# Performance work log

Measured on AMD Instinct MI355X. Metric: run time of the kernel, lower is better.

The kernel has to match this reference:

```python
import math
import jax, jax.numpy as jnp
import numpy as np

D_MODEL = 256
D2 = 2 * D_MODEL
NHEADS = 8
NLAYERS = 6
FFN = 1024
Q, B, S = 300, 16, 1024


def _ln(x, eps=1e-5):
    m = jnp.mean(x, axis=-1, keepdims=True)
    v = jnp.mean((x - m) ** 2, axis=-1, keepdims=True)
    return (x - m) / jnp.sqrt(v + eps)


def _mlp2(x, W1, b1, W2, b2):
    return jnp.maximum(x @ W1 + b1, 0.0) @ W2 + b2


def _sine_embed(pos, d_model):
    # pos: [Q, B, 2] -> [Q, B, d_model]
    fd = d_model // 2
    dim_t = jnp.arange(fd, dtype=jnp.float32)
    dim_t = 10000.0 ** (2.0 * jnp.floor(dim_t / 2.0) / fd)
    scale = 2.0 * math.pi
    px = (pos[:, :, 0] * scale)[:, :, None] / dim_t
    py = (pos[:, :, 1] * scale)[:, :, None] / dim_t

    def inter(p):
        q, b, _ = p.shape
        return jnp.stack((jnp.sin(p[:, :, 0::2]), jnp.cos(p[:, :, 1::2])), axis=3).reshape(q, b, -1)

    return jnp.concatenate((inter(py), inter(px)), axis=2)


def _pairwise_iou(b):
    # b: [B, Q, 4] xyxy -> [B, Q, Q]
    area = (b[..., 2] - b[..., 0]) * (b[..., 3] - b[..., 1])
    lt = jnp.maximum(b[:, :, None, :2], b[:, None, :, :2])
    rb = jnp.minimum(b[:, :, None, 2:], b[:, None, :, 2:])
    wh = jnp.clip(rb - lt, 0.0)
    inter = wh[..., 0] * wh[..., 1]
    union = area[:, :, None] + area[:, None, :] - inter
    return inter / union


def _mha(q, k, v, Wq, Wk, Wv, Wo, bias=None):
    # q: [L,B,D], k/v: [S,B,D]
    L, Bb, D = q.shape
    Ss = k.shape[0]
    hd = D // NHEADS
    qh = (q @ Wq).reshape(L, Bb, NHEADS, hd).transpose(1, 2, 0, 3)  # [B,H,L,hd]
    kh = (k @ Wk).reshape(Ss, Bb, NHEADS, hd).transpose(1, 2, 0, 3)
    vh = (v @ Wv).reshape(Ss, Bb, NHEADS, hd).transpose(1, 2, 0, 3)
    logits = jnp.einsum('bhqd,bhkd->bhqk', qh, kh) / jnp.sqrt(jnp.float32(hd))
    if bias is not None:
        logits = logits + bias[:, None]  # broadcast over heads
    a = jax.nn.softmax(logits, axis=-1)
    o = jnp.einsum('bhqk,bhkd->bhqd', a, vh).transpose(2, 0, 1, 3).reshape(L, Bb, D)
    return o @ Wo


def setup_inputs() -> dict:
    key = jax.random.key(0)
    ks = iter(jax.random.split(key, 40))
    f32 = jnp.float32
    d = D_MODEL
    sc = 0.02
    inp = {
        'tgt': jax.random.normal(next(ks), (Q, B, D2), f32),
        'memory': jax.random.normal(next(ks), (S, B, D2), f32),
        'pos': jax.random.normal(next(ks), (S, B, D2), f32),
        'query_pos': jax.random.normal(next(ks), (Q, B, d), f32),
        # query_scale MLP (d->d->d)
        'qs_W1': jax.random.normal(next(ks), (d, d), f32) * sc, 'qs_b1': jnp.zeros((d,), f32),
        'qs_W2': jax.random.normal(next(ks), (d, d), f32) * sc, 'qs_b2': jnp.zeros((d,), f32),
        # ref_point_head MLP (d->d->2)
        'rp_W1': jax.random.normal(next(ks), (d, d), f32) * sc, 'rp_b1': jnp.zeros((d,), f32),
        'rp_W2': jax.random.normal(next(ks), (d, 2), f32) * sc, 'rp_b2': jnp.zeros((2,), f32),
        # bbox_embed_func MLP (d->d->4)
        'bb_W1': jax.random.normal(next(ks), (d, d), f32) * sc, 'bb_b1': jnp.zeros((d,), f32),
        'bb_W2': jax.random.normal(next(ks), (d, 4), f32) * sc, 'bb_b2': jnp.zeros((4,), f32),
    }
    for name in ['sa_Wq', 'sa_Wk', 'sa_Wv', 'sa_Wo', 'ca_Wq', 'ca_Wk', 'ca_Wv', 'ca_Wo']:
        inp[name] = jax.random.normal(next(ks), (NLAYERS, D2, D2), f32) * sc
    inp['ff_W1'] = jax.random.normal(next(ks), (NLAYERS, D2, FFN), f32) * sc
    inp['ff_b1'] = jnp.zeros((NLAYERS, FFN), f32)
    inp['ff_W2'] = jax.random.normal(next(ks), (NLAYERS, FFN, D2), f32) * sc
    inp['ff_b2'] = jnp.zeros((NLAYERS, D2), f32)
    return inp


def reference(tgt, memory, pos, query_pos,
              qs_W1, qs_b1, qs_W2, qs_b2,
              rp_W1, rp_b1, rp_W2, rp_b2,
              bb_W1, bb_b1, bb_W2, bb_b2,
              sa_Wq, sa_Wk, sa_Wv, sa_Wo,
              ca_Wq, ca_Wk, ca_Wv, ca_Wo,
              ff_W1, ff_b1, ff_W2, ff_b2):
    d = D_MODEL
    output = tgt
    ref_before = _mlp2(query_pos, rp_W1, rp_b1, rp_W2, rp_b2)          # [Q,B,2]
    reference_points = jax.nn.sigmoid(ref_before).transpose(1, 0, 2)   # [B,Q,2]
    qp2 = jnp.concatenate((query_pos, query_pos), axis=-1)             # [Q,B,2d]
    for l in range(NLAYERS):
        obj_center = reference_points.transpose(1, 0, 2)               # [Q,B,2]
        pos_transform = _mlp2(output[..., d:], qs_W1, qs_b1, qs_W2, qs_b2)
        qs = _sine_embed(obj_center, d) * pos_transform                # [Q,B,d]
        tmp = _mlp2(output[..., d:], bb_W1, bb_b1, bb_W2, bb_b2)       # [Q,B,4]
        tmp = tmp.at[..., :2].add(ref_before)
        coord = jax.nn.sigmoid(tmp)                                    # cxcywh
        cx, cy, w, h = coord[..., 0], coord[..., 1], coord[..., 2], coord[..., 3]
        boxes = jnp.stack((cx - 0.5 * w, cy - 0.5 * h, cx + 0.5 * w, cy + 0.5 * h),
                          axis=-1).transpose(1, 0, 2)                  # [B,Q,4]
        gious = jax.lax.stop_gradient(_pairwise_iou(boxes))            # [B,Q,Q]
        cs = (cx + cy).transpose(1, 0)                                 # [B,Q]
        cxcys = jax.lax.stop_gradient((cs[:, :, None] > cs[:, None, :]).astype(output.dtype))
        bias = gious + cxcys                                            # [B,Q,Q]
        qs2 = jnp.concatenate((qs, qs), axis=-1)                        # [Q,B,2d]
        # self-attention with giou/cxcy bias
        qsa = output + qp2
        sa = _mha(qsa, qsa, output, sa_Wq[l], sa_Wk[l], sa_Wv[l], sa_Wo[l], bias=bias)
        output = _ln(output + sa)
        # cross-attention, sine-modulated query
        ca = _mha(output + qp2 + qs2, memory + pos, memory,
                  ca_Wq[l], ca_Wk[l], ca_Wv[l], ca_Wo[l])
        output = _ln(output + ca)
        ff = jnp.maximum(output @ ff_W1[l] + ff_b1[l], 0.0) @ ff_W2[l] + ff_b2[l]
        output = _ln(output + ff)
    return output[None]  # [1,Q,B,2d]
```

## Files before the change

kernel.cpp:

```cpp
#include <hip/hip_runtime.h>
#include <cmath>

#define QLEN 300
#define BATCH 16
#define SLEN 1024
#define DM 256
#define DD 512
#define FFND 1024
#define NQROWS (QLEN*BATCH)
#define NMROWS (SLEN*BATCH)
#define LQPAD 304
#define SAKPAD 320

typedef __attribute__((ext_vector_type(8))) short short8;
typedef __attribute__((ext_vector_type(4))) float f32x4;
typedef __attribute__((ext_vector_type(4))) unsigned short ushort4_;

__device__ __forceinline__ float sigmoidf_(float x){ return 1.f/(1.f+expf(-x)); }

__device__ __forceinline__ unsigned short f2bf(float x){
  unsigned u = __float_as_uint(x);
  unsigned r = (u + 0x7FFFu + ((u >> 16) & 1u)) >> 16;
  return (unsigned short)r;
}
__device__ __forceinline__ float bf2f(unsigned short u){
  return __uint_as_float(((unsigned)u) << 16);
}

__device__ __forceinline__ void gload16(const void* g, void* l) {
  __builtin_amdgcn_global_load_lds((const __attribute__((address_space(1))) unsigned int*)g,
                                   (__attribute__((address_space(3))) unsigned int*)l, 16, 0, 0);
}

__global__ __launch_bounds__(256) void transpose_cvt(
    const float* __restrict__ W, unsigned short* __restrict__ Wt, int K, int N,
    size_t zsrc, size_t zdst, float scale)
{
  __shared__ float T[32][33];
  int n0 = blockIdx.x*32, k0 = blockIdx.y*32;
  size_t zs = (size_t)blockIdx.z * zsrc;
  size_t zd = (size_t)blockIdx.z * zdst;
  int tx = threadIdx.x & 31, ty = threadIdx.x >> 5;
  #pragma unroll
  for (int j = 0; j < 32; j += 8)
    T[ty+j][tx] = W[zs + (size_t)(k0+ty+j)*N + n0+tx];
  __syncthreads();
  #pragma unroll
  for (int j = 0; j < 32; j += 8)
    Wt[zd + (size_t)(n0+ty+j)*K + k0+tx] = f2bf(T[tx][ty+j] * scale);
}

__global__ void concat_bias(const float* __restrict__ b1, const float* __restrict__ b2,
                            float* __restrict__ out)
{
  int i = blockIdx.x*256 + threadIdx.x;
  if (i < 256) out[i] = b1[i];
  else if (i < 512) out[i] = b2[i-256];
}

template<int BM, int OUTMODE, bool RELU>
__global__ __launch_bounds__(256) void gemm2(
    const unsigned short* __restrict__ Ab, const unsigned short* __restrict__ Wt,
    const float* __restrict__ bias, void* __restrict__ Cptr,
    int M, int N, int K, int lda, int Laux)
{
  __shared__ __align__(16) unsigned short As[2][BM*64];
  __shared__ __align__(16) unsigned short Bs[2][128*64];
  const int tid = threadIdx.x;
  const int w = tid >> 6, lane = tid & 63;
  const int bm = blockIdx.y*BM, bn = blockIdx.x*128;
  const int wm = w >> 1, wn = w & 1;
  const int c = lane & 15, hi = lane >> 4;
  constexpr int MR = (BM + 31)/32 < 1 ? 1 : BM/32;
  f32x4 acc[MR < 1 ? 1 : MR][4] = {};
  const int lrow8 = lane >> 3;
  const int lcol  = ((lane & 7) ^ lrow8) << 3;
  const int nt = K >> 6;

  auto stage = [&](int buf, int k0) {
    #pragma unroll
    for (int it = 0; it < BM/32; ++it) {
      int r = it*32 + w*8;
      gload16(&Ab[(size_t)(bm + r + lrow8)*lda + k0 + lcol], &As[buf][r*64]);
    }
    #pragma unroll
    for (int it = 0; it < 4; ++it) {
      int r = it*32 + w*8;
      gload16(&Wt[(size_t)(bn + r + lrow8)*K + k0 + lcol], &Bs[buf][r*64]);
    }
  };

  stage(0, 0);
  for (int t = 0; t < nt; ++t) {
    const int cur = t & 1;
    if (t + 1 < nt) {
      stage(cur ^ 1, (t+1) << 6);
      if constexpr (BM == 32)      asm volatile("s_waitcnt vmcnt(5)" ::: "memory");
      else if constexpr (BM == 64) asm volatile("s_waitcnt vmcnt(6)" ::: "memory");
      else                         asm volatile("s_waitcnt vmcnt(8)" ::: "memory");
    } else {
      asm volatile("s_waitcnt vmcnt(0)" ::: "memory");
    }
    __builtin_amdgcn_s_barrier();
    #pragma unroll
    for (int ks = 0; ks < 2; ++ks) {
      short8 a[MR], bf[4];
      #pragma unroll
      for (int mr = 0; mr < MR; ++mr) {
        int m = wm*(BM/2) + mr*16 + c;
        a[mr] = *reinterpret_cast<const short8*>(&As[cur][m*64 + ((ks*32 + hi*8) ^ ((m&7)<<3))]);
      }
      #pragma unroll
      for (int nr = 0; nr < 4; ++nr) {
        int n = wn*64 + nr*16 + c;
        bf[nr] = *reinterpret_cast<const short8*>(&Bs[cur][n*64 + ((ks*32 + hi*8) ^ ((n&7)<<3))]);
      }
      #pragma unroll
      for (int mr = 0; mr < MR; ++mr)
        #pragma unroll
        for (int nr = 0; nr < 4; ++nr)
          acc[mr][nr] = __builtin_amdgcn_mfma_f32_16x16x32_bf16(a[mr], bf[nr], acc[mr][nr], 0, 0, 0);
    }
    asm volatile("s_waitcnt lgkmcnt(0)" ::: "memory");
    __builtin_amdgcn_sched_barrier(0);
    __builtin_amdgcn_s_barrier();
  }
  const int hs = N >> 6;
  #pragma unroll
  for (int mr = 0; mr < MR; ++mr) {
    #pragma unroll
    for (int nr = 0; nr < 4; ++nr) {
      int colg = bn + wn*64 + nr*16 + c;
      float bv = bias ? bias[colg] : 0.f;
      #pragma unroll
      for (int r = 0; r < 4; ++r) {
        int rowg = bm + wm*(BM/2) + mr*16 + hi*4 + r;
        float v = acc[mr][nr][r] + bv;
        if (RELU) v = fmaxf(v, 0.f);
        if (OUTMODE == 0) {
          ((float*)Cptr)[(size_t)rowg*N + colg] = v;
        } else if (OUTMODE == 1) {
          ((unsigned short*)Cptr)[(size_t)rowg*N + colg] = f2bf(v);
        } else {
          int bb = rowg & 15, row = rowg >> 4, h = colg >> 6, dl = colg & 63;
          ((unsigned short*)Cptr)[(((size_t)bb*hs + h)*Laux + row)*64 + dl] = f2bf(v);
        }
      }
    }
  }
}

template<int BM>
__global__ __launch_bounds__(256) void gemm2_vt(
    const unsigned short* __restrict__ Ab, const unsigned short* __restrict__ Wt,
    unsigned short* __restrict__ VT, int Lsrc, int K, int lda, int Lkpad, int tilesPerB)
{
  __shared__ __align__(16) unsigned short As[2][BM*64];
  __shared__ __align__(16) unsigned short Bs[2][128*64];
  const int tid = threadIdx.x;
  const int w = tid >> 6, lane = tid & 63;
  const int b = blockIdx.y / tilesPerB;
  const int qt = (blockIdx.y - b*tilesPerB) * BM;
  const int bn = blockIdx.x*128;
  const int wm = w >> 1, wn = w & 1;
  const int c = lane & 15, hi = lane >> 4;
  constexpr int MR = BM/32;
  f32x4 acc[MR][4] = {};
  const int lrow8 = lane >> 3;
  const int lcol  = ((lane & 7) ^ lrow8) << 3;
  const int nt = K >> 6;

  auto stage = [&](int buf, int k0) {
    #pragma unroll
    for (int it = 0; it < BM/32; ++it) {
      int r = it*32 + w*8;
      int q = qt + r + lrow8; if (q > Lsrc-1) q = Lsrc-1;
      gload16(&Ab[(size_t)(q*BATCH + b)*lda + k0 + lcol], &As[buf][r*64]);
    }
    #pragma unroll
    for (int it = 0; it < 4; ++it) {
      int r = it*32 + w*8;
      gload16(&Wt[(size_t)(bn + r + lrow8)*K + k0 + lcol], &Bs[buf][r*64]);
    }
  };

  stage(0, 0);
  for (int t = 0; t < nt; ++t) {
    const int cur = t & 1;
    if (t + 1 < nt) {
      stage(cur ^ 1, (t+1) << 6);
      if constexpr (BM == 64) asm volatile("s_waitcnt vmcnt(6)" ::: "memory");
      else                    asm volatile("s_waitcnt vmcnt(8)" ::: "memory");
    } else {
      asm volatile("s_waitcnt vmcnt(0)" ::: "memory");
    }
    __builtin_amdgcn_s_barrier();
    #pragma unroll
    for (int ks = 0; ks < 2; ++ks) {
      short8 a[MR], bf[4];
      #pragma unroll
      for (int mr = 0; mr < MR; ++mr) {
        int m = wm*(BM/2) + mr*16 + c;
        a[mr] = *reinterpret_cast<const short8*>(&As[cur][m*64 + ((ks*32 + hi*8) ^ ((m&7)<<3))]);
      }
      #pragma unroll
      for (int nr = 0; nr < 4; ++nr) {
        int n = wn*64 + nr*16 + c;
        bf[nr] = *reinterpret_cast<const short8*>(&Bs[cur][n*64 + ((ks*32 + hi*8) ^ ((n&7)<<3))]);
      }
      #pragma unroll
      for (int mr = 0; mr < MR; ++mr)
        #pragma unroll
        for (int nr = 0; nr < 4; ++nr)
          acc[mr][nr] = __builtin_amdgcn_mfma_f32_16x16x32_bf16(a[mr], bf[nr], acc[mr][nr], 0, 0, 0);
    }
    asm volatile("s_waitcnt lgkmcnt(0)" ::: "memory");
    __builtin_amdgcn_sched_barrier(0);
    __builtin_amdgcn_s_barrier();
  }
  #pragma unroll
  for (int mr = 0; mr < MR; ++mr) {
    #pragma unroll
    for (int nr = 0; nr < 4; ++nr) {
      int colg = bn + wn*64 + nr*16 + c;
      int h = colg >> 6, dl = colg & 63;
      int q0 = qt + wm*(BM/2) + mr*16 + hi*4;
      ushort4_ pack;
      #pragma unroll
      for (int r = 0; r < 4; ++r) pack[r] = f2bf(acc[mr][nr][r]);
      *reinterpret_cast<ushort4_*>(&VT[((size_t)(b*8 + h)*64 + dl)*Lkpad + q0]) = pack;
    }
  }
}

__global__ __launch_bounds__(256) void gemm_mfma_split(
    const unsigned short* __restrict__ Ab, const unsigned short* __restrict__ Wt,
    const float* __restrict__ bias, unsigned short* __restrict__ C1, float* __restrict__ C2,
    int M, int N, int K, int lda)
{
  __shared__ __align__(16) unsigned short As[64][72];
  __shared__ __align__(16) unsigned short Bs[64][72];
  const int tid = threadIdx.x;
  const int bm = blockIdx.y*64, bn = blockIdx.x*64;
  const int w = tid >> 6, lane = tid & 63;
  const int wm = w >> 1, wn = w & 1;
  const int c = lane & 15, hi = lane >> 4;
  const int sr = tid >> 3, sk = (tid & 7) * 8;
  f32x4 acc[2][2] = {};
  for (int k0 = 0; k0 < K; k0 += 64) {
    #pragma unroll
    for (int it = 0; it < 2; ++it) {
      int m = sr + it*32;
      short8 v = *reinterpret_cast<const short8*>(&Ab[(size_t)(bm+m)*lda + k0 + sk]);
      *reinterpret_cast<short8*>(&As[m][sk]) = v;
      short8 bv = *reinterpret_cast<const short8*>(&Wt[(size_t)(bn+m)*K + k0 + sk]);
      *reinterpret_cast<short8*>(&Bs[m][sk]) = bv;
    }
    __syncthreads();
    #pragma unroll
    for (int ks = 0; ks < 2; ++ks) {
      short8 a0 = *reinterpret_cast<const short8*>(&As[wm*32 + c][ks*32 + hi*8]);
      short8 a1 = *reinterpret_cast<const short8*>(&As[wm*32 + 16 + c][ks*32 + hi*8]);
      short8 b0 = *reinterpret_cast<const short8*>(&Bs[wn*32 + c][ks*32 + hi*8]);
      short8 b1 = *reinterpret_cast<const short8*>(&Bs[wn*32 + 16 + c][ks*32 + hi*8]);
      acc[0][0] = __builtin_amdgcn_mfma_f32_16x16x32_bf16(a0, b0, acc[0][0], 0, 0, 0);
      acc[0][1] = __builtin_amdgcn_mfma_f32_16x16x32_bf16(a0, b1, acc[0][1], 0, 0, 0);
      acc[1][0] = __builtin_amdgcn_mfma_f32_16x16x32_bf16(a1, b0, acc[1][0], 0, 0, 0);
      acc[1][1] = __builtin_amdgcn_mfma_f32_16x16x32_bf16(a1, b1, acc[1][1], 0, 0, 0);
    }
    __syncthreads();
  }
  #pragma unroll
  for (int mf = 0; mf < 2; ++mf) {
    #pragma unroll
    for (int nf = 0; nf < 2; ++nf) {
      int colg = bn + wn*32 + nf*16 + c;
      float bv = bias[colg];
      #pragma unroll
      for (int r = 0; r < 4; ++r) {
        int rowg = bm + wm*32 + mf*16 + hi*4 + r;
        float v = fmaxf(acc[mf][nf][r] + bv, 0.f);
        if (colg < 256) C1[(size_t)rowg*256 + colg] = f2bf(v);
        else            C2[(size_t)rowg*256 + (colg-256)] = v;
      }
    }
  }
}

template<bool HAS_BIAS, bool MASK, int NS>
__global__ __launch_bounds__(256) void attn2(
    const unsigned short* __restrict__ Qh, const unsigned short* __restrict__ Kh,
    const unsigned short* __restrict__ VT, const float* __restrict__ bias,
    unsigned short* __restrict__ Ob, unsigned short* __restrict__ Opart, float* __restrict__ MLpart,
    int Lq, int Lk, int Lkpad, int qmul, int kmul, int koff)
{
  __shared__ __align__(16) unsigned short Ks[2][64*64];
  __shared__ __align__(16) unsigned short Vs[2][64*64];
  __shared__ __align__(16) unsigned short Pl[4][16*64];
  const int tid = threadIdx.x;
  const int w = tid >> 6, lane = tid & 63;
  const int c = lane & 15, hi = lane >> 4;
  const int bh = blockIdx.x;
  const int qt = blockIdx.y * 64;
  const int sp = blockIdx.z;
  const int b = bh >> 3, h = bh & 7;
  const int lrow8 = lane >> 3;
  const int lcol  = ((lane & 7) ^ lrow8) << 3;

  const int nt_tot = (Lk + 63) >> 6;
  const int t0 = (nt_tot * sp) / NS;
  const int t1 = (nt_tot * (sp + 1)) / NS;

  int qrow = qt + w*16 + c; if (qrow > Lq-1) qrow = Lq-1;
  const unsigned short* qptr = Qh + ((size_t)(b*qmul + h)*Lq + qrow)*64;
  short8 qf0 = *reinterpret_cast<const short8*>(qptr + hi*8);
  short8 qf1 = *reinterpret_cast<const short8*>(qptr + 32 + hi*8);
  const size_t kbase = (size_t)(b*kmul + koff + h)*Lk;

  float m_ = -1e30f, l_ = 0.f;
  f32x4 accO[4] = {};
  const int qbase = qt + w*16 + hi*4;

  auto stageKV = [&](int buf, int kt) {
    #pragma unroll
    for (int it = 0; it < 2; ++it) {
      int r = it*32 + w*8;
      int kr = kt + r + lrow8; if (MASK && kr > Lk-1) kr = Lk-1;
      gload16(&Kh[(kbase + kr)*64 + lcol], &Ks[buf][r*64]);
    }
    #pragma unroll
    for (int it = 0; it < 2; ++it) {
      int r = it*32 + w*8;
      gload16(&VT[((size_t)bh*64 + r + lrow8)*Lkpad + kt + lcol], &Vs[buf][r*64]);
    }
  };

  stageKV(0, t0 << 6);
  for (int t = t0; t < t1; ++t) {
    const int cur = (t - t0) & 1;
    const int kt = t << 6;
    float4 bs4[4];
    if (HAS_BIAS) {
      #pragma unroll
      for (int g = 0; g < 4; ++g)
        bs4[g] = *reinterpret_cast<const float4*>(
            &bias[((size_t)b*Lq + qrow)*Lk + kt + g*16 + hi*4]);
    }
    if (t + 1 < t1) {
      stageKV(cur ^ 1, (t+1) << 6);
      asm volatile("s_waitcnt vmcnt(4)" ::: "memory");
    } else {
      asm volatile("s_waitcnt vmcnt(0)" ::: "memory");
    }
    __builtin_amdgcn_s_barrier();
    f32x4 s[4] = {};
    __builtin_amdgcn_s_setprio(1);
    #pragma unroll
    for (int g = 0; g < 4; ++g) {
      int m = g*16 + c;
      short8 kb0 = *reinterpret_cast<const short8*>(&Ks[cur][m*64 + ((hi*8)      ^ ((m&7)<<3))]);
      short8 kb1 = *reinterpret_cast<const short8*>(&Ks[cur][m*64 + ((32 + hi*8) ^ ((m&7)<<3))]);
      s[g] = __builtin_amdgcn_mfma_f32_16x16x32_bf16(kb0, qf0, s[g], 0, 0, 0);
      s[g] = __builtin_amdgcn_mfma_f32_16x16x32_bf16(kb1, qf1, s[g], 0, 0, 0);
    }
    __builtin_amdgcn_s_setprio(0);
    float tmax = -1e30f;
    #pragma unroll
    for (int g = 0; g < 4; ++g) {
      #pragma unroll
      for (int r = 0; r < 4; ++r) {
        float v = s[g][r];
        if (HAS_BIAS) v += ((const float*)&bs4[g])[r];
        if (MASK && (kt + g*16 + hi*4 + r >= Lk)) v = -1e30f;
        s[g][r] = v;
        tmax = fmaxf(tmax, v);
      }
    }
    tmax = fmaxf(tmax, __shfl_xor(tmax, 16));
    tmax = fmaxf(tmax, __shfl_xor(tmax, 32));
    if (!__all(tmax - m_ <= 8.f)) {
      float newm = fmaxf(m_, tmax);
      float corr = __expf(m_ - newm);
      m_ = newm;
      l_ *= corr;
      float corr4[4];
      #pragma unroll
      for (int r = 0; r < 4; ++r) corr4[r] = __shfl(corr, hi*4 + r);
      #pragma unroll
      for (int dg = 0; dg < 4; ++dg)
        #pragma unroll
        for (int r = 0; r < 4; ++r) accO[dg][r] *= corr4[r];
    }
    float psum = 0.f;
    #pragma unroll
    for (int g = 0; g < 4; ++g) {
      ushort4_ pp;
      #pragma unroll
      for (int r = 0; r < 4; ++r) {
        float e = __expf(s[g][r] - m_);
        psum += e;
        pp[r] = f2bf(e);
      }
      int idx = c*64 + ((((g<<1)|(hi>>1)) ^ (c&7))<<3) + ((hi&1)<<2);
      *reinterpret_cast<ushort4_*>(&Pl[w][idx]) = pp;
    }
    psum += __shfl_xor(psum, 16);
    psum += __shfl_xor(psum, 32);
    l_ += psum;
    __builtin_amdgcn_s_setprio(1);
    #pragma unroll
    for (int ks = 0; ks < 2; ++ks) {
      short8 pa = *reinterpret_cast<const short8*>(&Pl[w][c*64 + ((((ks<<2)|hi) ^ (c&7))<<3)]);
      #pragma unroll
      for (int dg = 0; dg < 4; ++dg) {
        int n = dg*16 + c;
        short8 vb = *reinterpret_cast<const short8*>(&Vs[cur][n*64 + ((ks*32 + hi*8) ^ ((n&7)<<3))]);
        accO[dg] = __builtin_amdgcn_mfma_f32_16x16x32_bf16(pa, vb, accO[dg], 0, 0, 0);
      }
    }
    __builtin_amdgcn_s_setprio(0);
    asm volatile("s_waitcnt lgkmcnt(0)" ::: "memory");
    __builtin_amdgcn_sched_barrier(0);
    __builtin_amdgcn_s_barrier();
  }
  if (NS == 1) {
    float l4[4];
    #pragma unroll
    for (int r = 0; r < 4; ++r) l4[r] = __shfl(l_, hi*4 + r);
    #pragma unroll
    for (int r = 0; r < 4; ++r) {
      int qg = qbase + r;
      if (qg < Lq) {
        float inv = 1.f / l4[r];
        #pragma unroll
        for (int dg = 0; dg < 4; ++dg)
          Ob[((size_t)qg*BATCH + b)*DD + h*64 + 16*dg + c] = f2bf(accO[dg][r] * inv);
      }
    }
  } else {
    int qc = qt + w*16 + c;
    if (hi == 0 && qc < Lq) {
      size_t rowml = ((size_t)sp*128 + bh)*LQPAD + qc;
      MLpart[rowml*2]     = m_;
      MLpart[rowml*2 + 1] = l_;
    }
    #pragma unroll
    for (int r = 0; r < 4; ++r) {
      int qg = qbase + r;
      if (qg < Lq) {
        size_t rowo = ((size_t)sp*128 + bh)*LQPAD + qg;
        #pragma unroll
        for (int dg = 0; dg < 4; ++dg)
          Opart[rowo*64 + dg*16 + c] = f2bf(accO[dg][r]);
      }
    }
  }
}

template<int NSR>
__global__ __launch_bounds__(256) void attn_reduce(
    const unsigned short* __restrict__ Opart, const float* __restrict__ MLpart,
    unsigned short* __restrict__ Ob, int Lq)
{
  int w = threadIdx.x >> 6, lane = threadIdx.x & 63;
  int pair = blockIdx.x*4 + w;
  if (pair >= 128*Lq) return;
  int bh = pair / Lq, q = pair - bh*Lq;
  size_t rr[NSR];
  float m[NSR], l[NSR], M = -1e30f;
  #pragma unroll
  for (int s = 0; s < NSR; ++s) {
    rr[s] = ((size_t)s*128 + bh)*LQPAD + q;
    m[s] = MLpart[rr[s]*2];
    l[s] = MLpart[rr[s]*2 + 1];
    M = fmaxf(M, m[s]);
  }
  float o = 0.f, L = 0.f;
  #pragma unroll
  for (int s = 0; s < NSR; ++s) {
    float wg = __expf(m[s] - M);
    o += wg * bf2f(Opart[rr[s]*64 + lane]);
    L += wg * l[s];
  }
  int b = bh >> 3, h = bh & 7;
  Ob[((size_t)q*BATCH + b)*DD + h*64 + lane] = f2bf(o / L);
}

__global__ __launch_bounds__(256) void gemm_f32(
    const float* __restrict__ A, const float* __restrict__ A2,
    const float* __restrict__ W, const float* __restrict__ bias,
    float* __restrict__ C, int M, int N, int K, int lda, int relu)
{
  __shared__ __align__(16) float As[16][68];
  __shared__ __align__(16) float Bs[16][68];
  const int tid = threadIdx.x;
  const int bm = blockIdx.y * 64, bn = blockIdx.x * 64;
  const int tx = tid & 15, ty = tid >> 4;
  const int ar = tid >> 4, ac = tid & 15;
  const int bk = tid >> 6, bnn = tid & 63;
  float acc[4][4] = {};
  for (int k0 = 0; k0 < K; k0 += 16) {
    #pragma unroll
    for (int i = 0; i < 4; ++i) {
      int row = ar + i*16;
      float v = A[(size_t)(bm+row)*lda + (k0+ac)];
      if (A2) v += A2[(size_t)(bm+row)*lda + (k0+ac)];
      As[ac][row] = v;
    }
    #pragma unroll
    for (int i = 0; i < 4; ++i) {
      int kk = bk + i*4;
      Bs[kk][bnn] = W[(size_t)(k0+kk)*N + (bn+bnn)];
    }
    __syncthreads();
    #pragma unroll
    for (int k = 0; k < 16; ++k) {
      float4 a4 = *reinterpret_cast<const float4*>(&As[k][ty*4]);
      float4 b4 = *reinterpret_cast<const float4*>(&Bs[k][tx*4]);
      float a[4] = {a4.x,a4.y,a4.z,a4.w};
      float bb[4] = {b4.x,b4.y,b4.z,b4.w};
      #pragma unroll
      for (int i=0;i<4;++i)
        #pragma unroll
        for (int j=0;j<4;++j)
          acc[i][j] = fmaf(a[i], bb[j], acc[i][j]);
    }
    __syncthreads();
  }
  float vb[4] = {0.f,0.f,0.f,0.f};
  if (bias) {
    float4 b4 = *reinterpret_cast<const float4*>(&bias[bn + tx*4]);
    vb[0]=b4.x; vb[1]=b4.y; vb[2]=b4.z; vb[3]=b4.w;
  }
  #pragma unroll
  for (int i=0;i<4;++i) {
    int row = bm + ty*4 + i;
    float r0 = acc[i][0]+vb[0], r1 = acc[i][1]+vb[1], r2 = acc[i][2]+vb[2], r3 = acc[i][3]+vb[3];
    if (relu){ r0=fmaxf(r0,0.f); r1=fmaxf(r1,0.f); r2=fmaxf(r2,0.f); r3=fmaxf(r3,0.f); }
    float4 o; o.x=r0; o.y=r1; o.z=r2; o.w=r3;
    *reinterpret_cast<float4*>(&C[(size_t)row*N + bn + tx*4]) = o;
  }
}

__global__ __launch_bounds__(256) void gemm_skinny(
    const float* __restrict__ A, const float* __restrict__ W, const float* __restrict__ bias,
    float* __restrict__ C, int M, int N, int K, int lda)
{
  int wid = threadIdx.x >> 6, lane = threadIdx.x & 63;
  int row = blockIdx.x * 4 + wid;
  if (row >= M) return;
  float acc[4] = {0.f,0.f,0.f,0.f};
  for (int k = lane; k < K; k += 64) {
    float av = A[(size_t)row*lda + k];
    for (int n = 0; n < N; ++n) acc[n] += av * W[(size_t)k*N + n];
  }
  for (int off = 32; off; off >>= 1)
    for (int n = 0; n < N; ++n) acc[n] += __shfl_down(acc[n], off);
  if (lane == 0)
    for (int n = 0; n < N; ++n) C[(size_t)row*N + n] = acc[n] + bias[n];
}

__global__ void sine_embed_kernel(const float* __restrict__ refb, float* __restrict__ sine)
{
  int idx = blockIdx.x*blockDim.x + threadIdx.x;
  if (idx >= NQROWS*DM) return;
  int r = idx >> 8, c = idx & 255;
  int j = c & 127;
  float coord = refb[r*2 + (c < 128 ? 1 : 0)];
  float s = sigmoidf_(coord);
  float freq = expf(-(float)(j >> 1) * (9.210340371976184f / 64.f));
  float v = s * 6.283185307179586f * freq;
  sine[idx] = (j & 1) ? cosf(v) : sinf(v);
}

__global__ void boxes_kernel(const float* __restrict__ t4, const float* __restrict__ refb,
                             float* __restrict__ boxes, float* __restrict__ cs)
{
  int idx = blockIdx.x*blockDim.x + threadIdx.x;
  if (idx >= NQROWS) return;
  int q = idx / BATCH, b = idx % BATCH;
  float cx = sigmoidf_(t4[idx*4+0] + refb[idx*2+0]);
  float cy = sigmoidf_(t4[idx*4+1] + refb[idx*2+1]);
  float w  = sigmoidf_(t4[idx*4+2]);
  float h  = sigmoidf_(t4[idx*4+3]);
  int o = b*QLEN + q;
  boxes[o*4+0] = cx - 0.5f*w;
  boxes[o*4+1] = cy - 0.5f*h;
  boxes[o*4+2] = cx + 0.5f*w;
  boxes[o*4+3] = cy + 0.5f*h;
  cs[o] = cx + cy;
}

__global__ void bias_kernel(const float* __restrict__ boxes, const float* __restrict__ cs,
                            float* __restrict__ bias)
{
  int idx = blockIdx.x*blockDim.x + threadIdx.x;
  const int QQ = QLEN*QLEN;
  if (idx >= BATCH*QQ) return;
  int b = idx / QQ, rem = idx - b*QQ;
  int i = rem / QLEN, j = rem - i*QLEN;
  float4 bi = *reinterpret_cast<const float4*>(&boxes[((size_t)b*QLEN + i)*4]);
  float4 bj = *reinterpret_cast<const float4*>(&boxes[((size_t)b*QLEN + j)*4]);
  float ai = (bi.z-bi.x)*(bi.w-bi.y);
  float aj = (bj.z-bj.x)*(bj.w-bj.y);
  float ltx = fmaxf(bi.x, bj.x), lty = fmaxf(bi.y, bj.y);
  float rbx = fminf(bi.z, bj.z), rby = fminf(bi.w, bj.w);
  float w = fmaxf(rbx-ltx, 0.f), h = fmaxf(rby-lty, 0.f);
  float inter = w*h;
  float iou = inter / (ai + aj - inter);
  bias[idx] = iou + ((cs[b*QLEN+i] > cs[b*QLEN+j]) ? 1.f : 0.f);
}

__global__ void cvt_mem(const float* __restrict__ mem, const float* __restrict__ pos,
                        unsigned short* __restrict__ mb, unsigned short* __restrict__ mvb)
{
  int i = blockIdx.x*blockDim.x + threadIdx.x;
  if (i >= NMROWS*DD/8) return;
  size_t base = (size_t)i*8;
  float4 a0 = *reinterpret_cast<const float4*>(mem+base);
  float4 a1 = *reinterpret_cast<const float4*>(mem+base+4);
  float4 p0 = *reinterpret_cast<const float4*>(pos+base);
  float4 p1 = *reinterpret_cast<const float4*>(pos+base+4);
  short8 s1, s2;
  s1[0]=(short)f2bf(a0.x+p0.x); s1[1]=(short)f2bf(a0.y+p0.y); s1[2]=(short)f2bf(a0.z+p0.z); s1[3]=(short)f2bf(a0.w+p0.w);
  s1[4]=(short)f2bf(a1.x+p1.x); s1[5]=(short)f2bf(a1.y+p1.y); s1[6]=(short)f2bf(a1.z+p1.z); s1[7]=(short)f2bf(a1.w+p1.w);
  s2[0]=(short)f2bf(a0.x); s2[1]=(short)f2bf(a0.y); s2[2]=(short)f2bf(a0.z); s2[3]=(short)f2bf(a0.w);
  s2[4]=(short)f2bf(a1.x); s2[5]=(short)f2bf(a1.y); s2[6]=(short)f2bf(a1.z); s2[7]=(short)f2bf(a1.w);
  *reinterpret_cast<short8*>(mb+base)  = s1;
  *reinterpret_cast<short8*>(mvb+base) = s2;
}

template<int EMIT>
__global__ __launch_bounds__(256) void ln_residual_t(
    float* __restrict__ X, const float* __restrict__ Y, unsigned short* __restrict__ Xb,
    const float* __restrict__ qp, const float* __restrict__ sine, const float* __restrict__ pt,
    unsigned short* __restrict__ QIN)
{
  int row = blockIdx.x, tid = threadIdx.x;
  size_t base = (size_t)row*DD;
  float v0 = X[base+tid]     + Y[base+tid];
  float v1 = X[base+tid+256] + Y[base+tid+256];
  float s = v0+v1, sq = v0*v0+v1*v1;
  for (int off = 32; off; off >>= 1) { s += __shfl_down(s,off); sq += __shfl_down(sq,off); }
  __shared__ float ss[4], ssq[4];
  int wid = tid>>6, lane = tid&63;
  if (lane==0){ ss[wid]=s; ssq[wid]=sq; }
  __syncthreads();
  if (tid==0){
    float a=ss[0]+ss[1]+ss[2]+ss[3], bsum=ssq[0]+ssq[1]+ssq[2]+ssq[3];
    float mean = a*(1.f/DD);
    float var  = bsum*(1.f/DD) - mean*mean;
    ss[0]=mean; ssq[0]=rsqrtf(fmaxf(var,0.f)+1e-5f);
  }
  __syncthreads();
  float mean = ss[0], inv = ssq[0];
  float o0 = (v0-mean)*inv, o1 = (v1-mean)*inv;
  X[base+tid]     = o0;  Xb[base+tid]     = f2bf(o0);
  X[base+tid+256] = o1;  Xb[base+tid+256] = f2bf(o1);
  if (EMIT >= 1) {
    size_t c2 = (size_t)row*256 + tid;
    float add = qp[c2];
    if (EMIT == 2) add += sine[c2]*pt[c2];
    QIN[base+tid]     = f2bf(o0 + add);
    QIN[base+tid+256] = f2bf(o1 + add);
  }
}

__global__ void init_x(const float* __restrict__ t, const float* __restrict__ qp,
                       float* __restrict__ X, unsigned short* __restrict__ Xb,
                       unsigned short* __restrict__ QIN, int n)
{
  int idx = blockIdx.x*blockDim.x + threadIdx.x;
  if (idx < n){
    float v = t[idx]; X[idx]=v; Xb[idx]=f2bf(v);
    int r = idx >> 9, c = idx & 511;
    QIN[idx] = f2bf(v + qp[(r<<8) + (c & 255)]);
  }
}

__global__ void copy_f32(const float* __restrict__ src, float* __restrict__ dst, int n)
{
  int idx = blockIdx.x*blockDim.x + threadIdx.x;
  if (idx < n) dst[idx] = src[idx];
}

extern "C" void kernel_launch(void* const* d_in, const int* in_sizes, int n_in,
                              void* d_out, int out_size, void* d_ws, size_t ws_size,
                              hipStream_t stream)
{
  const float* tgt       = (const float*)d_in[0];
  const float* memory    = (const float*)d_in[1];
  const float* pos       = (const float*)d_in[2];
  const float* query_pos = (const float*)d_in[3];
  const float* qs_W1 = (const float*)d_in[4];  const float* qs_b1 = (const float*)d_in[5];
  const float* qs_W2 = (const float*)d_in[6];  const float* qs_b2 = (const float*)d_in[7];
  const float* rp_W1 = (const float*)d_in[8];  const float* rp_b1 = (const float*)d_in[9];
  const float* rp_W2 = (const float*)d_in[10]; const float* rp_b2 = (const float*)d_in[11];
  const float* bb_W1 = (const float*)d_in[12]; const float* bb_b1 = (const float*)d_in[13];
  const float* bb_W2 = (const float*)d_in[14]; const float* bb_b2 = (const float*)d_in[15];
  const float* sa_Wq = (const float*)d_in[16]; const float* sa_Wk = (const float*)d_in[17];
  const float* sa_Wv = (const float*)d_in[18]; const float* sa_Wo = (const float*)d_in[19];
  const float* ca_Wq = (const float*)d_in[20]; const float* ca_Wk = (const float*)d_in[21];
  const float* ca_Wv = (const float*)d_in[22]; const float* ca_Wo = (const float*)d_in[23];
  const float* ff_W1 = (const float*)d_in[24]; const float* ff_b1 = (const float*)d_in[25];
  const float* ff_W2 = (const float*)d_in[26]; const float* ff_b2 = (const float*)d_in[27];

  float* F = (float*)d_ws;
  size_t o = 0;
  float* X    = F + o; o += (size_t)NQROWS*DD;
  float* RES  = F + o; o += (size_t)NQROWS*DD;
  float* SINE = F + o; o += (size_t)NQROWS*DM;
  float* PT   = F + o; o += (size_t)NQROWS*DM;
  float* BIAS = F + o; o += (size_t)BATCH*QLEN*QLEN;
  float* REFB = F + o; o += (size_t)NQROWS*2;
  float* T4   = F + o; o += (size_t)NQROWS*4;
  float* BOX  = F + o; o += (size_t)NQROWS*4;
  float* CS   = F + o; o += (size_t)NQROWS;
  float* ML   = F + o; o += (size_t)2*128*LQPAD*2;
  float* QBB  = F + o; o += 512;
  float* T256 = RES;
  unsigned short* U = (unsigned short*)(F + o);
  size_t u = 0;
  unsigned short* Xb   = U + u; u += (size_t)NQROWS*DD;
  unsigned short* QIN  = U + u; u += (size_t)NQROWS*DD;
  unsigned short* PQb  = U + u; u += (size_t)NQROWS*DD;
  unsigned short* PKb  = U + u; u += (size_t)NMROWS*DD;
  unsigned short* PVb  = U + u; u += (size_t)NMROWS*DD;
  unsigned short* VTsa = U + u; u += (size_t)128*64*SAKPAD;
  unsigned short* OPARTU = U + u; u += (size_t)2*128*LQPAD*64;
  unsigned short* T256b= U + u; u += (size_t)NQROWS*DM;
  unsigned short* MEMb = U + u; u += (size_t)NMROWS*DD;
  unsigned short* MEMVb= U + u; u += (size_t)NMROWS*DD;
  unsigned short* WtSqk= U + u; u += (size_t)6*2*DD*DD;
  unsigned short* WtSv = U + u; u += (size_t)6*DD*DD;
  unsigned short* WtSo = U + u; u += (size_t)6*DD*DD;
  unsigned short* WtCq = U + u; u += (size_t)6*DD*DD;
  unsigned short* WtCk = U + u; u += (size_t)6*DD*DD;
  unsigned short* WtCv = U + u; u += (size_t)6*DD*DD;
  unsigned short* WtCo = U + u; u += (size_t)6*DD*DD;
  unsigned short* WtF1 = U + u; u += (size_t)6*DD*FFND;
  unsigned short* WtF2 = U + u; u += (size_t)6*DD*FFND;
  unsigned short* WtQB = U + u; u += (size_t)2*DM*DM;
  unsigned short* WtQ2 = U + u; u += (size_t)DM*DM;
  unsigned short* QKb  = PQb;
  unsigned short* AOb  = QIN;
  unsigned short* HIDb = PKb;
  if (ws_size < o*sizeof(float) + u*sizeof(unsigned short)) return;

  dim3 B256(256);
  const int nTotal = NQROWS*DD;
  const size_t ZD = (size_t)DD*DD;
  const size_t ZM = (size_t)DM*DM;

  transpose_cvt<<<dim3(16,16,6), B256, 0, stream>>>(sa_Wq, WtSqk,      DD, DD, ZD, 2*ZD, 0.125f);
  transpose_cvt<<<dim3(16,16,6), B256, 0, stream>>>(sa_Wk, WtSqk + ZD, DD, DD, ZD, 2*ZD, 1.f);
  transpose_cvt<<<dim3(16,16,6), B256, 0, stream>>>(sa_Wv, WtSv, DD, DD, ZD, ZD, 1.f);
  transpose_cvt<<<dim3(16,16,6), B256, 0, stream>>>(sa_Wo, WtSo, DD, DD, ZD, ZD, 1.f);
  transpose_cvt<<<dim3(16,16,6), B256, 0, stream>>>(ca_Wq, WtCq, DD, DD, ZD, ZD, 0.125f);
  transpose_cvt<<<dim3(16,16,6), B256, 0, stream>>>(ca_Wk, WtCk, DD, DD, ZD, ZD, 1.f);
  transpose_cvt<<<dim3(16,16,6), B256, 0, stream>>>(ca_Wv, WtCv, DD, DD, ZD, ZD, 1.f);
  transpose_cvt<<<dim3(16,16,6), B256, 0, stream>>>(ca_Wo, WtCo, DD, DD, ZD, ZD, 1.f);
  transpose_cvt<<<dim3(32,16,6), B256, 0, stream>>>(ff_W1, WtF1, DD, FFND, (size_t)DD*FFND, (size_t)DD*FFND, 1.f);
  transpose_cvt<<<dim3(16,32,6), B256, 0, stream>>>(ff_W2, WtF2, FFND, DD, (size_t)DD*FFND, (size_t)DD*FFND, 1.f);
  transpose_cvt<<<dim3(8,8,1),  B256, 0, stream>>>(qs_W1, WtQB,      DM, DM, ZM, ZM, 1.f);
  transpose_cvt<<<dim3(8,8,1),  B256, 0, stream>>>(bb_W1, WtQB + ZM, DM, DM, ZM, ZM, 1.f);
  transpose_cvt<<<dim3(8,8,1),  B256, 0, stream>>>(qs_W2, WtQ2, DM, DM, ZM, ZM, 1.f);
  concat_bias<<<dim3(2), B256, 0, stream>>>(qs_b1, bb_b1, QBB);

  init_x<<<dim3((nTotal+255)/256), B256, 0, stream>>>(tgt, query_pos, X, Xb, QIN, nTotal);
  cvt_mem<<<dim3(NMROWS*DD/8/256), B256, 0, stream>>>(memory, pos, MEMb, MEMVb);
  gemm_f32<<<dim3(DM/64, NQROWS/64), B256, 0, stream>>>(query_pos, nullptr, rp_W1, rp_b1, T256, NQROWS, DM, DM, DM, 1);
  gemm_skinny<<<dim3(NQROWS/4), B256, 0, stream>>>(T256, rp_W2, rp_b2, REFB, NQROWS, 2, DM, DM);
  sine_embed_kernel<<<dim3((NQROWS*DM+255)/256), B256, 0, stream>>>(REFB, SINE);

  const int nredu = (128*QLEN + 3) / 4;
  const int qtiles = (QLEN + 63) / 64;
  for (int l = 0; l < 6; ++l) {
    const size_t wo = (size_t)l*DD*DD, fo = (size_t)l*DD*FFND;
    const float* fb1 = ff_b1 + (size_t)l*FFND;
    const float* fb2 = ff_b2 + (size_t)l*DD;

    gemm_mfma_split<<<dim3(8, NQROWS/64), B256, 0, stream>>>(Xb+DM, WtQB, QBB, T256b, T256, NQROWS, 512, DM, DD);
    gemm2<32,0,false><<<dim3(DM/128, NQROWS/32), B256, 0, stream>>>(T256b, WtQ2, qs_b2, PT, NQROWS, DM, DM, DM, 0);
    gemm_skinny<<<dim3(NQROWS/4), B256, 0, stream>>>(T256, bb_W2, bb_b2, T4, NQROWS, 4, DM, DM);
    boxes_kernel<<<dim3((NQROWS+255)/256), B256, 0, stream>>>(T4, REFB, BOX, CS);
    bias_kernel<<<dim3((BATCH*QLEN*QLEN+255)/256), B256, 0, stream>>>(BOX, CS, BIAS);

    gemm2<64,2,false><<<dim3(1024/128, NQROWS/64), B256, 0, stream>>>(QIN, WtSqk + (size_t)l*2*ZD, nullptr, QKb, NQROWS, 1024, DD, DD, QLEN);
    gemm2_vt<64><<<dim3(DD/128, BATCH*5), B256, 0, stream>>>(Xb, WtSv+wo, VTsa, QLEN, DD, DD, SAKPAD, 5);
    attn2<true,true,2><<<dim3(128, qtiles, 2), B256, 0, stream>>>(QKb, QKb, VTsa, BIAS, nullptr, OPARTU, ML, QLEN, QLEN, SAKPAD, 16, 16, 8);
    attn_reduce<2><<<dim3(nredu), B256, 0, stream>>>(OPARTU, ML, AOb, QLEN);
    gemm2<32,0,false><<<dim3(DD/128, NQROWS/32), B256, 0, stream>>>(AOb, WtSo+wo, nullptr, RES, NQROWS, DD, DD, DD, 0);
    ln_residual_t<2><<<dim3(NQROWS), B256, 0, stream>>>(X, RES, Xb, query_pos, SINE, PT, QIN);

    gemm2<32,2,false><<<dim3(DD/128, NQROWS/32), B256, 0, stream>>>(QIN, WtCq+wo, nullptr, PQb, NQROWS, DD, DD, DD, QLEN);
    gemm2<128,2,false><<<dim3(DD/128, NMROWS/128), B256, 0, stream>>>(MEMb,  WtCk+wo, nullptr, PKb, NMROWS, DD, DD, DD, SLEN);
    gemm2_vt<128><<<dim3(DD/128, BATCH*8), B256, 0, stream>>>(MEMVb, WtCv+wo, PVb, SLEN, DD, DD, SLEN, 8);
    attn2<false,false,2><<<dim3(128, qtiles, 2), B256, 0, stream>>>(PQb, PKb, PVb, nullptr, nullptr, OPARTU, ML, QLEN, SLEN, SLEN, 8, 8, 0);
    attn_reduce<2><<<dim3(nredu), B256, 0, stream>>>(OPARTU, ML, AOb, QLEN);
    gemm2<32,0,false><<<dim3(DD/128, NQROWS/32), B256, 0, stream>>>(AOb, WtCo+wo, nullptr, RES, NQROWS, DD, DD, DD, 0);
    ln_residual_t<0><<<dim3(NQROWS), B256, 0, stream>>>(X, RES, Xb, nullptr, nullptr, nullptr, nullptr);

    gemm2<64,1,true ><<<dim3(FFND/128, NQROWS/64), B256, 0, stream>>>(Xb, WtF1+fo, fb1, HIDb, NQROWS, FFND, DD, DD, 0);
    gemm2<32,0,false><<<dim3(DD/128, NQROWS/32), B256, 0, stream>>>(HIDb, WtF2+fo, fb2, RES, NQROWS, DD, FFND, FFND, 0);
    ln_residual_t<1><<<dim3(NQROWS), B256, 0, stream>>>(X, RES, Xb, query_pos, nullptr, nullptr, QIN);
  }

  copy_f32<<<dim3((nTotal+255)/256), B256, 0, stream>>>(X, (float*)d_out, out_size);
}
```

Measured before the change: 1.572 ms.

## Use exp2 softmax, fuse box head into skinny GEMM, drop self-attn split

```diff
diff --git a/kernel.cpp b/kernel.cpp
--- a/kernel.cpp
+++ b/kernel.cpp
@@ -11,6 +11,7 @@
 #define NMROWS (SLEN*BATCH)
 #define LQPAD 304
 #define SAKPAD 320
+#define LOG2E 1.4426950408889634f
 
 typedef __attribute__((ext_vector_type(8))) short short8;
 typedef __attribute__((ext_vector_type(4))) float f32x4;
@@ -378,9 +379,9 @@
     }
     tmax = fmaxf(tmax, __shfl_xor(tmax, 16));
     tmax = fmaxf(tmax, __shfl_xor(tmax, 32));
-    if (!__all(tmax - m_ <= 8.f)) {
+    if (!__all(tmax - m_ <= 11.5416f)) {
       float newm = fmaxf(m_, tmax);
-      float corr = __expf(m_ - newm);
+      float corr = exp2f(m_ - newm);
       m_ = newm;
       l_ *= corr;
       float corr4[4];
@@ -397,7 +398,7 @@
       ushort4_ pp;
       #pragma unroll
       for (int r = 0; r < 4; ++r) {
-        float e = __expf(s[g][r] - m_);
+        float e = exp2f(s[g][r] - m_);
         psum += e;
         pp[r] = f2bf(e);
       }
@@ -478,7 +479,7 @@
   float o = 0.f, L = 0.f;
   #pragma unroll
   for (int s = 0; s < NSR; ++s) {
-    float wg = __expf(m[s] - M);
+    float wg = exp2f(m[s] - M);
     o += wg * bf2f(Opart[rr[s]*64 + lane]);
     L += wg * l[s];
   }
@@ -560,6 +561,38 @@
     for (int n = 0; n < N; ++n) C[(size_t)row*N + n] = acc[n] + bias[n];
 }
 
+__global__ __launch_bounds__(256) void gemm_skinny_boxes(
+    const float* __restrict__ A, const float* __restrict__ W, const float* __restrict__ bias,
+    const float* __restrict__ refb, float* __restrict__ boxes, float* __restrict__ cs,
+    int M, int K, int lda)
+{
+  int wid = threadIdx.x >> 6, lane = threadIdx.x & 63;
+  int row = blockIdx.x * 4 + wid;
+  if (row >= M) return;
+  float acc[4] = {0.f,0.f,0.f,0.f};
+  for (int k = lane; k < K; k += 64) {
+    float av = A[(size_t)row*lda + k];
+    #pragma unroll
+    for (int n = 0; n < 4; ++n) acc[n] += av * W[(size_t)k*4 + n];
+  }
+  for (int off = 32; off; off >>= 1)
+    #pragma unroll
+    for (int n = 0; n < 4; ++n) acc[n] += __shfl_down(acc[n], off);
+  if (lane == 0) {
+    int q = row / BATCH, b = row - q*BATCH;
+    float cx = sigmoidf_(acc[0] + bias[0] + refb[row*2+0]);
+    float cy = sigmoidf_(acc[1] + bias[1] + refb[row*2+1]);
+    float w_ = sigmoidf_(acc[2] + bias[2]);
+    float h_ = sigmoidf_(acc[3] + bias[3]);
+    int o = b*QLEN + q;
+    boxes[o*4+0] = cx - 0.5f*w_;
+    boxes[o*4+1] = cy - 0.5f*h_;
+    boxes[o*4+2] = cx + 0.5f*w_;
+    boxes[o*4+3] = cy + 0.5f*h_;
+    cs[o] = cx + cy;
+  }
+}
+
 __global__ void sine_embed_kernel(const float* __restrict__ refb, float* __restrict__ sine)
 {
   int idx = blockIdx.x*blockDim.x + threadIdx.x;
@@ -571,24 +604,6 @@
   float freq = expf(-(float)(j >> 1) * (9.210340371976184f / 64.f));
   float v = s * 6.283185307179586f * freq;
   sine[idx] = (j & 1) ? cosf(v) : sinf(v);
-}
-
-__global__ void boxes_kernel(const float* __restrict__ t4, const float* __restrict__ refb,
-                             float* __restrict__ boxes, float* __restrict__ cs)
-{
-  int idx = blockIdx.x*blockDim.x + threadIdx.x;
-  if (idx >= NQROWS) return;
-  int q = idx / BATCH, b = idx % BATCH;
-  float cx = sigmoidf_(t4[idx*4+0] + refb[idx*2+0]);
-  float cy = sigmoidf_(t4[idx*4+1] + refb[idx*2+1]);
-  float w  = sigmoidf_(t4[idx*4+2]);
-  float h  = sigmoidf_(t4[idx*4+3]);
-  int o = b*QLEN + q;
-  boxes[o*4+0] = cx - 0.5f*w;
-  boxes[o*4+1] = cy - 0.5f*h;
-  boxes[o*4+2] = cx + 0.5f*w;
-  boxes[o*4+3] = cy + 0.5f*h;
-  cs[o] = cx + cy;
 }
 
 __global__ void bias_kernel(const float* __restrict__ boxes, const float* __restrict__ cs,
@@ -608,7 +623,7 @@
   float w = fmaxf(rbx-ltx, 0.f), h = fmaxf(rby-lty, 0.f);
   float inter = w*h;
   float iou = inter / (ai + aj - inter);
-  bias[idx] = iou + ((cs[b*QLEN+i] > cs[b*QLEN+j]) ? 1.f : 0.f);
+  bias[idx] = (iou + ((cs[b*QLEN+i] > cs[b*QLEN+j]) ? 1.f : 0.f)) * LOG2E;
 }
 
 __global__ void cvt_mem(const float* __restrict__ mem, const float* __restrict__ pos,
@@ -713,7 +728,6 @@
   float* PT   = F + o; o += (size_t)NQROWS*DM;
   float* BIAS = F + o; o += (size_t)BATCH*QLEN*QLEN;
   float* REFB = F + o; o += (size_t)NQROWS*2;
-  float* T4   = F + o; o += (size_t)NQROWS*4;
   float* BOX  = F + o; o += (size_t)NQROWS*4;
   float* CS   = F + o; o += (size_t)NQROWS;
   float* ML   = F + o; o += (size_t)2*128*LQPAD*2;
@@ -751,12 +765,13 @@
   const int nTotal = NQROWS*DD;
   const size_t ZD = (size_t)DD*DD;
   const size_t ZM = (size_t)DM*DM;
-
-  transpose_cvt<<<dim3(16,16,6), B256, 0, stream>>>(sa_Wq, WtSqk,      DD, DD, ZD, 2*ZD, 0.125f);
+  const float QSC = 0.125f * LOG2E;
+
+  transpose_cvt<<<dim3(16,16,6), B256, 0, stream>>>(sa_Wq, WtSqk,      DD, DD, ZD, 2*ZD, QSC);
   transpose_cvt<<<dim3(16,16,6), B256, 0, stream>>>(sa_Wk, WtSqk + ZD, DD, DD, ZD, 2*ZD, 1.f);
   transpose_cvt<<<dim3(16,16,6), B256, 0, stream>>>(sa_Wv, WtSv, DD, DD, ZD, ZD, 1.f);
   transpose_cvt<<<dim3(16,16,6), B256, 0, stream>>>(sa_Wo, WtSo, DD, DD, ZD, ZD, 1.f);
-  transpose_cvt<<<dim3(16,16,6), B256, 0, stream>>>(ca_Wq, WtCq, DD, DD, ZD, ZD, 0.125f);
+  transpose_cvt<<<dim3(16,16,6), B256, 0, stream>>>(ca_Wq, WtCq, DD, DD, ZD, ZD, QSC);
   transpose_cvt<<<dim3(16,16,6), B256, 0, stream>>>(ca_Wk, WtCk, DD, DD, ZD, ZD, 1.f);
   transpose_cvt<<<dim3(16,16,6), B256, 0, stream>>>(ca_Wv, WtCv, DD, DD, ZD, ZD, 1.f);
   transpose_cvt<<<dim3(16,16,6), B256, 0, stream>>>(ca_Wo, WtCo, DD, DD, ZD, ZD, 1.f);
@@ -782,14 +797,12 @@
 
     gemm_mfma_split<<<dim3(8, NQROWS/64), B256, 0, stream>>>(Xb+DM, WtQB, QBB, T256b, T256, NQROWS, 512, DM, DD);
     gemm2<32,0,false><<<dim3(DM/128, NQROWS/32), B256, 0, stream>>>(T256b, WtQ2, qs_b2, PT, NQROWS, DM, DM, DM, 0);
-    gemm_skinny<<<dim3(NQROWS/4), B256, 0, stream>>>(T256, bb_W2, bb_b2, T4, NQROWS, 4, DM, DM);
-    boxes_kernel<<<dim3((NQROWS+255)/256), B256, 0, stream>>>(T4, REFB, BOX, CS);
+    gemm_skinny_boxes<<<dim3(NQROWS/4), B256, 0, stream>>>(T256, bb_W2, bb_b2, REFB, BOX, CS, NQROWS, DM, DM);
     bias_kernel<<<dim3((BATCH*QLEN*QLEN+255)/256), B256, 0, stream>>>(BOX, CS, BIAS);
 
     gemm2<64,2,false><<<dim3(1024/128, NQROWS/64), B256, 0, stream>>>(QIN, WtSqk + (size_t)l*2*ZD, nullptr, QKb, NQROWS, 1024, DD, DD, QLEN);
     gemm2_vt<64><<<dim3(DD/128, BATCH*5), B256, 0, stream>>>(Xb, WtSv+wo, VTsa, QLEN, DD, DD, SAKPAD, 5);
-    attn2<true,true,2><<<dim3(128, qtiles, 2), B256, 0, stream>>>(QKb, QKb, VTsa, BIAS, nullptr, OPARTU, ML, QLEN, QLEN, SAKPAD, 16, 16, 8);
-    attn_reduce<2><<<dim3(nredu), B256, 0, stream>>>(OPARTU, ML, AOb, QLEN);
+    attn2<true,true,1><<<dim3(128, qtiles, 1), B256, 0, stream>>>(QKb, QKb, VTsa, BIAS, AOb, OPARTU, ML, QLEN, QLEN, SAKPAD, 16, 16, 8);
     gemm2<32,0,false><<<dim3(DD/128, NQROWS/32), B256, 0, stream>>>(AOb, WtSo+wo, nullptr, RES, NQROWS, DD, DD, DD, 0);
     ln_residual_t<2><<<dim3(NQROWS), B256, 0, stream>>>(X, RES, Xb, query_pos, SINE, PT, QIN);
 
```

Measured after the change: 1.510 ms. -3.9%, faster.
